# Optimization experiments

Hardware: AMD Instinct MI355X
Metric: run time of the kernel (lower is better)

The kernel has to match this reference:

```python
import jax, jax.numpy as jnp
import numpy as np

B, T, C, H = 4, 2048, 1024, 16
D = C // H  # head_dim = 64

def setup_inputs() -> dict:
    key = jax.random.key(0)
    k1, k2, k3 = jax.random.split(key, 3)
    x = jax.random.normal(k1, (B, T, C), dtype=jnp.float32)
    # Linear weights stored as (out_features, in_features) like torch; we apply x @ W.T
    w_attn = jax.random.normal(k2, (3 * C, C), dtype=jnp.float32) * (1.0 / np.sqrt(C))
    w_proj = jax.random.normal(k3, (C, C), dtype=jnp.float32) * (1.0 / np.sqrt(C))
    return {"x": x, "w_attn": w_attn, "w_proj": w_proj}

def reference(x, w_attn, w_proj):
    Bv, Tv, Cv = x.shape
    qkv = jnp.einsum('btc,fc->btf', x, w_attn)  # [B,T,3C]
    q, k, v = jnp.split(qkv, 3, axis=-1)
    # [B,H,T,D]
    q = q.reshape(Bv, Tv, H, D).transpose(0, 2, 1, 3)
    k = k.reshape(Bv, Tv, H, D).transpose(0, 2, 1, 3)
    v = v.reshape(Bv, Tv, H, D).transpose(0, 2, 1, 3)
    scale = 1.0 / np.sqrt(D).astype(np.float32)
    att = jnp.einsum('bhqd,bhkd->bhqk', q, k) * scale
    causal = jnp.tril(jnp.ones((Tv, Tv), dtype=bool))
    att = jnp.where(causal, att, -jnp.inf)
    att = jax.nn.softmax(att, axis=-1)
    y = jnp.einsum('bhqk,bhkd->bhqd', att, v)
    y = y.transpose(0, 2, 1, 3).reshape(Bv, Tv, Cv)
    return jnp.einsum('btc,oc->bto', y, w_proj)
```

## Files before the change

### kernel.cpp

```cpp
#include <hip/hip_runtime.h>
#include <cstdint>
#include <cstddef>

typedef __attribute__((ext_vector_type(8))) short short8;
typedef __attribute__((ext_vector_type(4))) float f32x4;
typedef unsigned int u32;

#define MFMA_BF16(a, b, c) __builtin_amdgcn_mfma_f32_16x16x32_bf16((a), (b), (c), 0, 0, 0)

__device__ __forceinline__ void async16(const void* g, void* l) {
  __builtin_amdgcn_global_load_lds(
      (const __attribute__((address_space(1))) u32*)g,
      (__attribute__((address_space(3))) u32*)l, 16, 0, 0);
}

__device__ __forceinline__ short f2bf(float f) {
  u32 u = __builtin_bit_cast(u32, f);
  u += 0x7fffu + ((u >> 16) & 1u);
  return (short)(u >> 16);
}

__device__ __forceinline__ u32 pack_bf16_trunc(float lo, float hi) {
  return __builtin_amdgcn_perm(__builtin_bit_cast(u32, hi),
                               __builtin_bit_cast(u32, lo), 0x07060302u);
}

__global__ void cast_bf16_kernel(const float* __restrict__ in,
                                 short* __restrict__ out, int n4) {
  int i = blockIdx.x * blockDim.x + threadIdx.x;
  if (i < n4) {
    float4 v = ((const float4*)in)[i];
    short4 r;
    r.x = f2bf(v.x); r.y = f2bf(v.y); r.z = f2bf(v.z); r.w = f2bf(v.w);
    ((short4*)out)[i] = r;
  }
}

__global__ void cast_wattn_kernel(const float* __restrict__ in,
                                  short* __restrict__ out, int n4) {
  int i = blockIdx.x * blockDim.x + threadIdx.x;
  if (i < n4) {
    const float sc = (i * 4 < 1024 * 1024) ? 0.18033688011112042f : 1.0f;
    float4 v = ((const float4*)in)[i];
    short4 r;
    r.x = f2bf(v.x * sc); r.y = f2bf(v.y * sc);
    r.z = f2bf(v.z * sc); r.w = f2bf(v.w * sc);
    ((short4*)out)[i] = r;
  }
}

template <bool OUT_BF16>
__global__ __launch_bounds__(256) void gemm_bt_kernel(
    const short* __restrict__ A, const short* __restrict__ Bt,
    void* __restrict__ Cv, int M, int N, int K) {
  __shared__ __align__(16) short As[128 * 32];
  __shared__ __align__(16) short Bs[128 * 32];

  const int tid  = threadIdx.x;
  const int lane = tid & 63;
  const int wave = tid >> 6;
  const int quad = lane >> 4;
  const int l15  = lane & 15;

  const int id  = blockIdx.y * gridDim.x + blockIdx.x;
  const int xcd = id & 7;
  const int j   = id >> 3;
  const int by  = xcd * 8 + (j & 7);
  const int bx  = j >> 3;
  const int bm  = by * 128;
  const int bn  = bx * 128;

  const int wm = (wave >> 1) * 64;
  const int wn = (wave & 1) * 64;

  f32x4 acc[4][4];
#pragma unroll
  for (int i = 0; i < 4; ++i)
#pragma unroll
    for (int jj = 0; jj < 4; ++jj) acc[i][jj] = (f32x4){0.f, 0.f, 0.f, 0.f};

  const int s0 = tid, s1 = tid + 256;
  const int r0 = s0 >> 2, c0 = (s0 & 3) ^ ((s0 >> 3) & 3);
  const int r1 = s1 >> 2, c1 = (s1 & 3) ^ ((s1 >> 3) & 3);
  const short* ga0 = A  + (size_t)(bm + r0) * K + c0 * 8;
  const short* ga1 = A  + (size_t)(bm + r1) * K + c1 * 8;
  const short* gb0 = Bt + (size_t)(bn + r0) * K + c0 * 8;
  const short* gb1 = Bt + (size_t)(bn + r1) * K + c1 * 8;

  const int xr = (l15 >> 1) & 3;

  for (int k0 = 0; k0 < K; k0 += 32) {
    __syncthreads();
    async16(ga0 + k0, &As[s0 * 8]);
    async16(ga1 + k0, &As[s1 * 8]);
    async16(gb0 + k0, &Bs[s0 * 8]);
    async16(gb1 + k0, &Bs[s1 * 8]);
    __syncthreads();

    short8 af[4], bf[4];
#pragma unroll
    for (int mt = 0; mt < 4; ++mt)
      af[mt] = *(const short8*)&As[(wm + mt * 16 + l15) * 32 + (quad ^ xr) * 8];
#pragma unroll
    for (int nt = 0; nt < 4; ++nt)
      bf[nt] = *(const short8*)&Bs[(wn + nt * 16 + l15) * 32 + (quad ^ xr) * 8];
#pragma unroll
    for (int mt = 0; mt < 4; ++mt)
#pragma unroll
      for (int nt = 0; nt < 4; ++nt)
        acc[mt][nt] = MFMA_BF16(af[mt], bf[nt], acc[mt][nt]);
  }

#pragma unroll
  for (int mt = 0; mt < 4; ++mt) {
    const int r0e = bm + wm + mt * 16 + quad * 4;
#pragma unroll
    for (int nt = 0; nt < 4; ++nt) {
      const int c = bn + wn + nt * 16 + l15;
#pragma unroll
      for (int reg = 0; reg < 4; ++reg) {
        float v = acc[mt][nt][reg];
        if (OUT_BF16)
          ((short*)Cv)[(size_t)(r0e + reg) * N + c] = f2bf(v);
        else
          ((float*)Cv)[(size_t)(r0e + reg) * N + c] = v;
      }
    }
  }
}

__global__ __launch_bounds__(256) void vtrans_kernel(
    const short* __restrict__ qkv, short* __restrict__ vt) {
  __shared__ __align__(16) short Ts[64 * 80];
  const int t0 = blockIdx.x * 64;
  const int bh = blockIdx.y;
  const int b = bh >> 4, h = bh & 15;
  const int tid = threadIdx.x;
#pragma unroll
  for (int it = 0; it < 2; ++it) {
    const int ci = tid + it * 256;
    const int t = ci >> 3, cw = ci & 7;
    short8 v = *(const short8*)(qkv + (size_t)(b * 2048 + t0 + t) * 3072 +
                                2048 + h * 64 + cw * 8);
    *(short8*)&Ts[t * 80 + cw * 8] = v;
  }
  __syncthreads();
#pragma unroll
  for (int it = 0; it < 2; ++it) {
    const int ci = tid + it * 256;
    const int d = ci >> 3, c2 = ci & 7;
    short tmp[8];
#pragma unroll
    for (int j = 0; j < 8; ++j) tmp[j] = Ts[(c2 * 8 + j) * 80 + d];
    *(short8*)(vt + (size_t)(bh * 64 + d) * 2048 + t0 + c2 * 8) =
        *(short8*)tmp;
  }
}

__global__ __launch_bounds__(256, 2) void attn_kernel(
    const short* __restrict__ qkv, const short* __restrict__ vt,
    short* __restrict__ y) {
  __shared__ __align__(16) short Ks[2][4096];
  __shared__ __align__(16) short Vs[2][4096];
  __shared__ __align__(16) short Ps[4][1024];

  const int bh    = blockIdx.x;
  const int pairi = blockIdx.y;
  const int b = bh >> 4, h = bh & 15;
  const int tid  = threadIdx.x;
  const int lane = tid & 63;
  const int wave = tid >> 6;
  const int quad = lane >> 4, l15 = lane & 15;
  const int base_row = b * 2048;
  short* Pw = &Ps[wave][0];

  const int s0 = tid, s1 = tid + 256;
  const int r0s = s0 >> 3, c0s = (s0 & 7) ^ (r0s & 7);
  const int r1s = s1 >> 3, c1s = (s1 & 7) ^ (r1s & 7);
  const short* kbase0 = qkv + (size_t)(base_row + r0s) * 3072 + 1024 + h * 64 + c0s * 8;
  const short* kbase1 = qkv + (size_t)(base_row + r1s) * 3072 + 1024 + h * 64 + c1s * 8;
  const short* vbase0 = vt + (size_t)(bh * 64 + r0s) * 2048 + c0s * 8;
  const short* vbase1 = vt + (size_t)(bh * 64 + r1s) * 2048 + c1s * 8;

  const int xk = l15 & 7;

  for (int half = 0; half < 2; ++half) {
    const int qi  = half ? (15 - pairi) : pairi;
    const int r0  = qi * 128;
    const int nkt = 2 * qi + 2;
    const int qg0a = r0 + wave * 32;

    short8 qf[2][2];
#pragma unroll
    for (int g = 0; g < 2; ++g) {
      const short* qp = qkv +
          (size_t)(base_row + qg0a + g * 16 + l15) * 3072 + h * 64 + quad * 8;
      qf[g][0] = *(const short8*)qp;
      qf[g][1] = *(const short8*)(qp + 32);
    }
    float l_r[2] = {0.f, 0.f};
    f32x4 o[2][4];
#pragma unroll
    for (int g = 0; g < 2; ++g)
#pragma unroll
      for (int dt = 0; dt < 4; ++dt) o[g][dt] = (f32x4){0.f, 0.f, 0.f, 0.f};

    async16(kbase0, &Ks[0][s0 * 8]);
    async16(kbase1, &Ks[0][s1 * 8]);
    async16(vbase0, &Vs[0][s0 * 8]);
    async16(vbase1, &Vs[0][s1 * 8]);

    for (int kt = 0; kt < nkt; ++kt) {
      const int kvb = kt * 64;
      __syncthreads();

      if (kt + 1 < nkt) {
        const int nb = (kt + 1) & 1;
        const size_t koff = (size_t)(kvb + 64) * 3072;
        async16(kbase0 + koff, &Ks[nb][s0 * 8]);
        async16(kbase1 + koff, &Ks[nb][s1 * 8]);
        async16(vbase0 + kvb + 64, &Vs[nb][s0 * 8]);
        async16(vbase1 + kvb + 64, &Vs[nb][s1 * 8]);
      }
      const short* Kb = &Ks[kt & 1][0];
      const short* Vb = &Vs[kt & 1][0];

      short8 kf[4][2];
#pragma unroll
      for (int nt = 0; nt < 4; ++nt) {
        kf[nt][0] = *(const short8*)&Kb[(nt * 16 + l15) * 64 + ((quad) ^ xk) * 8];
        kf[nt][1] = *(const short8*)&Kb[(nt * 16 + l15) * 64 + ((4 + quad) ^ xk) * 8];
      }
      short8 vf[4][2];
#pragma unroll
      for (int dt = 0; dt < 4; ++dt) {
        vf[dt][0] = *(const short8*)&Vb[(dt * 16 + l15) * 64 + ((quad) ^ xk) * 8];
        vf[dt][1] = *(const short8*)&Vb[(dt * 16 + l15) * 64 + ((4 + quad) ^ xk) * 8];
      }

#pragma unroll
      for (int g = 0; g < 2; ++g) {
        const int qg0 = qg0a + g * 16;
        if (kvb > qg0 + 15) continue;

        f32x4 s[4];
#pragma unroll
        for (int nt = 0; nt < 4; ++nt) {
          s[nt] = MFMA_BF16(kf[nt][0], qf[g][0], ((f32x4){0.f, 0.f, 0.f, 0.f}));
          s[nt] = MFMA_BF16(kf[nt][1], qf[g][1], s[nt]);
        }

        float p[4][4];
        if (kvb + 64 <= qg0) {
#pragma unroll
          for (int nt = 0; nt < 4; ++nt)
#pragma unroll
            for (int r = 0; r < 4; ++r)
              p[nt][r] = __builtin_amdgcn_exp2f(s[nt][r]);
        } else {
          const int qrel = qg0 + l15 - kvb;
#pragma unroll
          for (int nt = 0; nt < 4; ++nt)
#pragma unroll
            for (int r = 0; r < 4; ++r) {
              const int kvl = nt * 16 + quad * 4 + r;
              p[nt][r] = (kvl <= qrel) ? __builtin_amdgcn_exp2f(s[nt][r]) : 0.f;
            }
        }

        float rs = ((p[0][0] + p[0][1]) + (p[0][2] + p[0][3])) +
                   ((p[1][0] + p[1][1]) + (p[1][2] + p[1][3])) +
                   ((p[2][0] + p[2][1]) + (p[2][2] + p[2][3])) +
                   ((p[3][0] + p[3][1]) + (p[3][2] + p[3][3]));
        rs += __shfl_xor(rs, 16);
        rs += __shfl_xor(rs, 32);
        l_r[g] += rs;

#pragma unroll
        for (int nt = 0; nt < 4; ++nt) {
          u32 w0 = pack_bf16_trunc(p[nt][0], p[nt][1]);
          u32 w1 = pack_bf16_trunc(p[nt][2], p[nt][3]);
          const int p0 = 8 * nt + 2 * quad;
          u32* dst = (u32*)Pw + (p0 >> 4) * 256 + ((p0 >> 2) & 3) * 64 +
                     l15 * 4 + (p0 & 3);
          *(uint2*)dst = make_uint2(w0, w1);
        }
        short8 pf0 = *(const short8*)&Pw[quad * 128 + l15 * 8];
        short8 pf1 = *(const short8*)&Pw[512 + quad * 128 + l15 * 8];

#pragma unroll
        for (int dt = 0; dt < 4; ++dt) {
          o[g][dt] = MFMA_BF16(vf[dt][0], pf0, o[g][dt]);
          o[g][dt] = MFMA_BF16(vf[dt][1], pf1, o[g][dt]);
        }
      }
    }

#pragma unroll
    for (int g = 0; g < 2; ++g) {
      const float inv = 1.f / l_r[g];
#pragma unroll
      for (int dt = 0; dt < 4; ++dt) {
        const int d = dt * 16 + quad * 4;
        u32 w0 = pack_bf16_trunc(o[g][dt][0] * inv, o[g][dt][1] * inv);
        u32 w1 = pack_bf16_trunc(o[g][dt][2] * inv, o[g][dt][3] * inv);
        *(uint2*)&Pw[(d >> 5) * 512 + l15 * 32 + (d & 31)] = make_uint2(w0, w1);
      }
      const int qq = lane >> 2, ck = lane & 3;
      const size_t yrow = (size_t)(base_row + qg0a + g * 16 + qq);
#pragma unroll
      for (int kkd = 0; kkd < 2; ++kkd) {
        short8 vv = *(const short8*)&Pw[kkd * 512 + qq * 32 + ck * 8];
        *(short8*)(y + yrow * 1024 + h * 64 + kkd * 32 + ck * 8) = vv;
      }
    }
    __syncthreads();
  }
}

extern "C" void kernel_launch(void* const* d_in, const int* in_sizes, int n_in,
                              void* d_out, int out_size, void* d_ws,
                              size_t ws_size, hipStream_t stream) {
  const float* x  = (const float*)d_in[0];
  const float* wa = (const float*)d_in[1];
  const float* wp = (const float*)d_in[2];
  float* out = (float*)d_out;

  char* ws = (char*)d_ws;
  short* xb  = (short*)(ws + 0);
  short* wab = (short*)(ws + 16777216);
  short* wpb = (short*)(ws + 23068672);
  short* qkv = (short*)(ws + 25165824);
  short* yb  = (short*)(ws + 75497472);
  short* vtb = xb;

  cast_bf16_kernel <<<8192, 256, 0, stream>>>(x,  xb,  8388608 / 4);
  cast_wattn_kernel<<<3072, 256, 0, stream>>>(wa, wab, 3145728 / 4);
  cast_bf16_kernel <<<1024, 256, 0, stream>>>(wp, wpb, 1048576 / 4);

  gemm_bt_kernel<true><<<dim3(3072 / 128, 8192 / 128), 256, 0, stream>>>(
      xb, wab, (void*)qkv, 8192, 3072, 1024);

  vtrans_kernel<<<dim3(32, 64), 256, 0, stream>>>(qkv, vtb);

  attn_kernel<<<dim3(64, 8), 256, 0, stream>>>(qkv, vtb, yb);

  gemm_bt_kernel<false><<<dim3(1024 / 128, 8192 / 128), 256, 0, stream>>>(
      yb, wpb, (void*)out, 8192, 1024, 1024);
}
```

Before: 261.5 us.

## Merge cast kernels into one launch and double GEMM K-tile to 64

Replaces three separate fp32-to-bf16 cast launches with a single kernel that dispatches on the global index. The GEMM now stages a 64-wide K slice per iteration instead of 32, using a matching XOR swizzle for the LDS reads. This halves the number of barrier pairs per GEMM and gives more MFMAs between syncs. In exchange it doubles LDS use per block, which may reduce occupancy, and it still has no double buffering.

Measured after the change: 247.2 us. 5.5% less time.

```diff
diff --git a/kernel.cpp b/kernel.cpp
--- a/kernel.cpp
+++ b/kernel.cpp
@@ -25,36 +25,40 @@
                                __builtin_bit_cast(u32, lo), 0x07060302u);
 }
 
-__global__ void cast_bf16_kernel(const float* __restrict__ in,
-                                 short* __restrict__ out, int n4) {
-  int i = blockIdx.x * blockDim.x + threadIdx.x;
-  if (i < n4) {
-    float4 v = ((const float4*)in)[i];
-    short4 r;
-    r.x = f2bf(v.x); r.y = f2bf(v.y); r.z = f2bf(v.z); r.w = f2bf(v.w);
-    ((short4*)out)[i] = r;
-  }
-}
-
-__global__ void cast_wattn_kernel(const float* __restrict__ in,
-                                  short* __restrict__ out, int n4) {
-  int i = blockIdx.x * blockDim.x + threadIdx.x;
-  if (i < n4) {
-    const float sc = (i * 4 < 1024 * 1024) ? 0.18033688011112042f : 1.0f;
-    float4 v = ((const float4*)in)[i];
-    short4 r;
-    r.x = f2bf(v.x * sc); r.y = f2bf(v.y * sc);
-    r.z = f2bf(v.z * sc); r.w = f2bf(v.w * sc);
-    ((short4*)out)[i] = r;
-  }
+__global__ __launch_bounds__(256) void cast_all_kernel(
+    const float* __restrict__ x, const float* __restrict__ wa,
+    const float* __restrict__ wp, short* __restrict__ xb,
+    short* __restrict__ wab, short* __restrict__ wpb) {
+  const int i = blockIdx.x * blockDim.x + threadIdx.x;
+  const float4* src;
+  short4* dst;
+  float sc = 1.0f;
+  if (i < 2097152) {
+    src = (const float4*)x + i;
+    dst = (short4*)xb + i;
+  } else if (i < 2883584) {
+    const int j = i - 2097152;
+    if (j < 262144) sc = 0.18033688011112042f;
+    src = (const float4*)wa + j;
+    dst = (short4*)wab + j;
+  } else {
+    const int j = i - 2883584;
+    src = (const float4*)wp + j;
+    dst = (short4*)wpb + j;
+  }
+  float4 v = *src;
+  short4 r;
+  r.x = f2bf(v.x * sc); r.y = f2bf(v.y * sc);
+  r.z = f2bf(v.z * sc); r.w = f2bf(v.w * sc);
+  *dst = r;
 }
 
 template <bool OUT_BF16>
 __global__ __launch_bounds__(256) void gemm_bt_kernel(
     const short* __restrict__ A, const short* __restrict__ Bt,
     void* __restrict__ Cv, int M, int N, int K) {
-  __shared__ __align__(16) short As[128 * 32];
-  __shared__ __align__(16) short Bs[128 * 32];
+  __shared__ __align__(16) short As[128 * 64];
+  __shared__ __align__(16) short Bs[128 * 64];
 
   const int tid  = threadIdx.x;
   const int lane = tid & 63;
@@ -79,36 +83,45 @@
 #pragma unroll
     for (int jj = 0; jj < 4; ++jj) acc[i][jj] = (f32x4){0.f, 0.f, 0.f, 0.f};
 
-  const int s0 = tid, s1 = tid + 256;
-  const int r0 = s0 >> 2, c0 = (s0 & 3) ^ ((s0 >> 3) & 3);
-  const int r1 = s1 >> 2, c1 = (s1 & 3) ^ ((s1 >> 3) & 3);
-  const short* ga0 = A  + (size_t)(bm + r0) * K + c0 * 8;
-  const short* ga1 = A  + (size_t)(bm + r1) * K + c1 * 8;
-  const short* gb0 = Bt + (size_t)(bn + r0) * K + c0 * 8;
-  const short* gb1 = Bt + (size_t)(bn + r1) * K + c1 * 8;
-
-  const int xr = (l15 >> 1) & 3;
-
-  for (int k0 = 0; k0 < K; k0 += 32) {
+  int srow[4], scol[4];
+#pragma unroll
+  for (int it = 0; it < 4; ++it) {
+    const int s = tid + it * 256;
+    srow[it] = s >> 3;
+    scol[it] = ((s & 7) ^ (srow[it] & 7)) * 8;
+  }
+  const int xk = l15 & 7;
+
+  for (int k0 = 0; k0 < K; k0 += 64) {
     __syncthreads();
-    async16(ga0 + k0, &As[s0 * 8]);
-    async16(ga1 + k0, &As[s1 * 8]);
-    async16(gb0 + k0, &Bs[s0 * 8]);
-    async16(gb1 + k0, &Bs[s1 * 8]);
+#pragma unroll
+    for (int it = 0; it < 4; ++it) {
+      const int s = tid + it * 256;
+      async16(A  + (size_t)(bm + srow[it]) * K + k0 + scol[it], &As[s * 8]);
+      async16(Bt + (size_t)(bn + srow[it]) * K + k0 + scol[it], &Bs[s * 8]);
+    }
     __syncthreads();
 
-    short8 af[4], bf[4];
-#pragma unroll
-    for (int mt = 0; mt < 4; ++mt)
-      af[mt] = *(const short8*)&As[(wm + mt * 16 + l15) * 32 + (quad ^ xr) * 8];
-#pragma unroll
-    for (int nt = 0; nt < 4; ++nt)
-      bf[nt] = *(const short8*)&Bs[(wn + nt * 16 + l15) * 32 + (quad ^ xr) * 8];
-#pragma unroll
-    for (int mt = 0; mt < 4; ++mt)
-#pragma unroll
-      for (int nt = 0; nt < 4; ++nt)
-        acc[mt][nt] = MFMA_BF16(af[mt], bf[nt], acc[mt][nt]);
+    short8 af[4][2], bf[4][2];
+#pragma unroll
+    for (int mt = 0; mt < 4; ++mt) {
+      const int ra = (wm + mt * 16 + l15) * 64;
+      af[mt][0] = *(const short8*)&As[ra + ((quad) ^ xk) * 8];
+      af[mt][1] = *(const short8*)&As[ra + ((4 + quad) ^ xk) * 8];
+    }
+#pragma unroll
+    for (int nt = 0; nt < 4; ++nt) {
+      const int rb = (wn + nt * 16 + l15) * 64;
+      bf[nt][0] = *(const short8*)&Bs[rb + ((quad) ^ xk) * 8];
+      bf[nt][1] = *(const short8*)&Bs[rb + ((4 + quad) ^ xk) * 8];
+    }
+#pragma unroll
+    for (int kk = 0; kk < 2; ++kk)
+#pragma unroll
+      for (int mt = 0; mt < 4; ++mt)
+#pragma unroll
+        for (int nt = 0; nt < 4; ++nt)
+          acc[mt][nt] = MFMA_BF16(af[mt][kk], bf[nt][kk], acc[mt][nt]);
   }
 
 #pragma unroll
@@ -334,9 +347,7 @@
   short* yb  = (short*)(ws + 75497472);
   short* vtb = xb;
 
-  cast_bf16_kernel <<<8192, 256, 0, stream>>>(x,  xb,  8388608 / 4);
-  cast_wattn_kernel<<<3072, 256, 0, stream>>>(wa, wab, 3145728 / 4);
-  cast_bf16_kernel <<<1024, 256, 0, stream>>>(wp, wpb, 1048576 / 4);
+  cast_all_kernel<<<12288, 256, 0, stream>>>(x, wa, wp, xb, wab, wpb);
 
   gemm_bt_kernel<true><<<dim3(3072 / 128, 8192 / 128), 256, 0, stream>>>(
       xb, wab, (void*)qkv, 8192, 3072, 1024);
```
